# Kernel tuning notes

Measured on AMD Instinct MI355X. Metric: run time of the kernel, lower is better.

## Reference

```python
import jax, jax.numpy as jnp
import numpy as np

B, S, D = 2, 2048, 1024
H = 16
HD = D // H
W = 256  # attention window half-width


def setup_inputs() -> dict:
    key = jax.random.key(0)
    ks = jax.random.split(key, 9)
    scale = 1.0 / np.sqrt(D)
    inp = {
        "x": jax.random.normal(ks[0], (B, S, D), dtype=jnp.float32),
        "Wq": jax.random.normal(ks[1], (D, D), dtype=jnp.float32) * scale,
        "bq": jnp.zeros((D,), dtype=jnp.float32),
        "Wk": jax.random.normal(ks[2], (D, D), dtype=jnp.float32) * scale,
        "bk": jnp.zeros((D,), dtype=jnp.float32),
        "Wv": jax.random.normal(ks[3], (D, D), dtype=jnp.float32) * scale,
        "bv": jnp.zeros((D,), dtype=jnp.float32),
        "Wo": jax.random.normal(ks[4], (D, D), dtype=jnp.float32) * scale,
        "bo": jnp.zeros((D,), dtype=jnp.float32),
    }
    return inp


def reference(x, Wq, bq, Wk, bk, Wv, bv, Wo, bo):
    # Linear projections (torch Linear: x @ W.T + b), split heads -> [B,H,S,HD]
    def proj(W, b):
        y = x @ W.T + b
        return y.reshape(B, S, H, HD).transpose(0, 2, 1, 3)

    q = proj(Wq, bq)
    k = proj(Wk, bk)
    v = proj(Wv, bv)

    scores = jnp.einsum("bhqd,bhkd->bhqk", q, k) / jnp.sqrt(
        jnp.asarray(HD, dtype=jnp.float32))

    # banded local mask: keep |i - j| <= W
    i = jnp.arange(S)[:, None]
    j = jnp.arange(S)[None, :]
    local_mask = jnp.abs(i - j) <= W  # [S,S] bool
    scores = jnp.where(local_mask[None, None], scores, -jnp.inf)

    attn = jax.nn.softmax(scores, axis=-1)  # [B,H,S,S]
    context = jnp.einsum("bhqk,bhkd->bhqd", attn, v)
    context = context.transpose(0, 2, 1, 3).reshape(B, S, D)
    out = context @ Wo.T + bo
    return (out, attn)
```

## Files before the change

### kernel.cpp

```cpp
#include <hip/hip_runtime.h>

#define B_ 2
#define S_ 2048
#define D_ 1024
#define H_ 16
#define HD_ 64
#define MSZ 4096

typedef __attribute__((ext_vector_type(8))) short short8;
typedef __attribute__((ext_vector_type(4))) float f32x4;
typedef unsigned short u16;

#define MFMA16(a, b, c) __builtin_amdgcn_mfma_f32_16x16x32_bf16((a), (b), (c), 0, 0, 0)

typedef __attribute__((address_space(1))) const unsigned int gu32;
typedef __attribute__((address_space(3))) unsigned int lu32;
#define STAGE16(gp, lp) \
  __builtin_amdgcn_global_load_lds((gu32*)(gp), (lu32*)(lp), 16, 0, 0)

__device__ __forceinline__ u16 f2bf(float f) {
  union { float f; unsigned u; } v; v.f = f;
  unsigned r = v.u + 0x7FFFu + ((v.u >> 16) & 1u);
  return (u16)(r >> 16);
}
__device__ __forceinline__ float bf2f(u16 h) {
  union { unsigned u; float f; } v; v.u = ((unsigned)h) << 16;
  return v.f;
}

__global__ void split_kernel(const float* __restrict__ x, const float* __restrict__ wq,
                             const float* __restrict__ wk, const float* __restrict__ wv,
                             const float* __restrict__ wo, u16* __restrict__ xh,
                             u16* __restrict__ xl, u16* __restrict__ wch,
                             u16* __restrict__ wcl, u16* __restrict__ woh,
                             u16* __restrict__ wol) {
  const size_t base = (size_t)blockIdx.x * 256 + threadIdx.x;
#pragma unroll
  for (int it = 0; it < 4; ++it) {
    const size_t v = base + (size_t)it * 524288;
    float4 f;
    u16 *dh, *dl;
    size_t off;
    if (v < 1048576) {
      f = ((const float4*)x)[v]; dh = xh; dl = xl; off = v;
    } else if (v < 1310720) {
      f = ((const float4*)wq)[v - 1048576]; dh = wch; dl = wcl; off = v - 1048576;
    } else if (v < 1572864) {
      f = ((const float4*)wk)[v - 1310720]; dh = wch; dl = wcl; off = v - 1048576;
    } else if (v < 1835008) {
      f = ((const float4*)wv)[v - 1572864]; dh = wch; dl = wcl; off = v - 1048576;
    } else {
      f = ((const float4*)wo)[v - 1835008]; dh = woh; dl = wol; off = v - 1835008;
    }
    const float e[4] = {f.x, f.y, f.z, f.w};
    u16 h4[4], l4[4];
#pragma unroll
    for (int q = 0; q < 4; ++q) {
      h4[q] = f2bf(e[q]);
      l4[q] = f2bf(e[q] - bf2f(h4[q]));
    }
    *(ushort4*)&dh[off * 4] = make_ushort4(h4[0], h4[1], h4[2], h4[3]);
    *(ushort4*)&dl[off * 4] = make_ushort4(l4[0], l4[1], l4[2], l4[3]);
  }
}

__global__ void split_ctx(const float* __restrict__ src, u16* __restrict__ dh,
                          u16* __restrict__ dl) {
  const size_t base = (size_t)blockIdx.x * 256 + threadIdx.x;
#pragma unroll
  for (int it = 0; it < 2; ++it) {
    const size_t v = base + (size_t)it * 524288;
    float4 f = ((const float4*)src)[v];
    const float e[4] = {f.x, f.y, f.z, f.w};
    u16 h4[4], l4[4];
#pragma unroll
    for (int q = 0; q < 4; ++q) {
      h4[q] = f2bf(e[q]);
      l4[q] = f2bf(e[q] - bf2f(h4[q]));
    }
    *(ushort4*)&dh[v * 4] = make_ushort4(h4[0], h4[1], h4[2], h4[3]);
    *(ushort4*)&dl[v * 4] = make_ushort4(l4[0], l4[1], l4[2], l4[3]);
  }
}

template <int EPI>
__global__ __launch_bounds__(256, 2) void gemm_bf(
    const u16* __restrict__ Ahg, const u16* __restrict__ Alg,
    const u16* __restrict__ Bhg, const u16* __restrict__ Blg,
    const float* __restrict__ b0, const float* __restrict__ b1,
    const float* __restrict__ b2, u16* __restrict__ oh, u16* __restrict__ ol,
    float* __restrict__ outf) {
  __shared__ u16 Ah[128 * 32], Al[128 * 32], Bh[128 * 32], Bl[128 * 32];
  const int tid = threadIdx.x, lane = tid & 63, wave = tid >> 6;
  const int wr = wave >> 1, wc = wave & 1;
  const int g = lane >> 4, ln = lane & 15;
  const int mbase = blockIdx.y * 128;
  const int nbase = blockIdx.x * 128;

  f32x4 acc[4][4];
  {
    f32x4 z = {0.f, 0.f, 0.f, 0.f};
#pragma unroll
    for (int i = 0; i < 4; ++i)
#pragma unroll
      for (int j = 0; j < 4; ++j) acc[i][j] = z;
  }

  const int srow = wave * 16 + (lane >> 2);
  const int scol = (lane & 3) * 8;
  const size_t a0 = (size_t)(mbase + srow) * 1024 + scol;
  const size_t a1 = a0 + (size_t)64 * 1024;
  const size_t bo0 = (size_t)(nbase + srow) * 1024 + scol;
  const size_t bo1 = bo0 + (size_t)64 * 1024;
  u16* const lA0 = &Ah[(wave * 16) * 32];
  u16* const lA1 = &Ah[(64 + wave * 16) * 32];
  u16* const lB0 = &Bh[(wave * 16) * 32];
  u16* const lB1 = &Bh[(64 + wave * 16) * 32];
  u16* const lA0l = &Al[(wave * 16) * 32];
  u16* const lA1l = &Al[(64 + wave * 16) * 32];
  u16* const lB0l = &Bl[(wave * 16) * 32];
  u16* const lB1l = &Bl[(64 + wave * 16) * 32];

  for (int kt = 0; kt < 32; ++kt) {
    const int k0 = kt * 32;
    STAGE16(Ahg + a0 + k0, lA0);
    STAGE16(Ahg + a1 + k0, lA1);
    STAGE16(Alg + a0 + k0, lA0l);
    STAGE16(Alg + a1 + k0, lA1l);
    STAGE16(Bhg + bo0 + k0, lB0);
    STAGE16(Bhg + bo1 + k0, lB1);
    STAGE16(Blg + bo0 + k0, lB0l);
    STAGE16(Blg + bo1 + k0, lB1l);
    __syncthreads();
    short8 af[4][2], bf[4][2];
#pragma unroll
    for (int mi = 0; mi < 4; ++mi) {
      const int r = wr * 64 + mi * 16 + ln;
      af[mi][0] = *(const short8*)&Ah[r * 32 + g * 8];
      af[mi][1] = *(const short8*)&Al[r * 32 + g * 8];
    }
#pragma unroll
    for (int ni = 0; ni < 4; ++ni) {
      const int r = wc * 64 + ni * 16 + ln;
      bf[ni][0] = *(const short8*)&Bh[r * 32 + g * 8];
      bf[ni][1] = *(const short8*)&Bl[r * 32 + g * 8];
    }
#pragma unroll
    for (int mi = 0; mi < 4; ++mi)
#pragma unroll
      for (int ni = 0; ni < 4; ++ni) {
        acc[mi][ni] = MFMA16(af[mi][0], bf[ni][0], acc[mi][ni]);
        acc[mi][ni] = MFMA16(af[mi][0], bf[ni][1], acc[mi][ni]);
        acc[mi][ni] = MFMA16(af[mi][1], bf[ni][0], acc[mi][ni]);
      }
    __syncthreads();
  }

  const size_t P = (size_t)B_ * H_ * S_ * HD_;
  if constexpr (EPI == 0) {
#pragma unroll
    for (int mi = 0; mi < 4; ++mi)
#pragma unroll
      for (int ni = 0; ni < 4; ++ni) {
        const int nl3 = nbase + wc * 64 + ni * 16 + ln;
        const int which = nl3 >> 10;
        const float* bp = (which == 0) ? b0 : (which == 1) ? b1 : b2;
        const float bv = bp[nl3 & 1023];
        const int hh = (nl3 >> 6) & 15, hd = nl3 & 63;
#pragma unroll
        for (int reg = 0; reg < 4; ++reg) {
          const int mm = mbase + wr * 64 + mi * 16 + g * 4 + reg;
          const int bb = mm >> 11, ss = mm & 2047;
          const size_t dst =
              (size_t)which * P + (((size_t)bb * 16 + hh) * 2048 + ss) * 64 + hd;
          const float val = acc[mi][ni][reg] + bv;
          const u16 hi = f2bf(val);
          oh[dst] = hi;
          ol[dst] = f2bf(val - bf2f(hi));
        }
      }
  } else {
#pragma unroll
    for (int mi = 0; mi < 4; ++mi)
#pragma unroll
      for (int ni = 0; ni < 4; ++ni) {
        const int nl = nbase + wc * 64 + ni * 16 + ln;
        const float bv = b0[nl];
#pragma unroll
        for (int reg = 0; reg < 4; ++reg) {
          const int mm = mbase + wr * 64 + mi * 16 + g * 4 + reg;
          outf[(size_t)mm * 1024 + nl] = acc[mi][ni][reg] + bv;
        }
      }
  }
}

__global__ __launch_bounds__(256, 2) void attn_kernel(
    const u16* __restrict__ qh, const u16* __restrict__ ql,
    const u16* __restrict__ kh, const u16* __restrict__ kl,
    const u16* __restrict__ vh, const u16* __restrict__ vl,
    float* __restrict__ attn, float* __restrict__ ctx) {
  __shared__ u16 Plds[32][584];
  __shared__ u16 Vth[64][136], Vtl[64][136];
  __shared__ float red[2][4][32];

  const int tid = threadIdx.x, lane = tid & 63, wave = tid >> 6;
  const int g = lane >> 4, ln = lane & 15;
  int bid = blockIdx.x;
  bid = (bid & 7) * 256 + (bid >> 3);
  const int bh = bid >> 6;
  const int qblk = bid & 63;
  const int b = bh >> 4, h = bh & 15;
  const int i0 = qblk * 32;
  const int j0 = i0 - 256;
  const size_t bh_off = (size_t)bh * S_ * HD_;
  const float NINF = -__builtin_inff();

  short8 qf[2][2][2];
#pragma unroll
  for (int mi = 0; mi < 2; ++mi)
#pragma unroll
    for (int ks = 0; ks < 2; ++ks) {
      const size_t off = bh_off + (size_t)(i0 + mi * 16 + ln) * 64 + ks * 32 + g * 8;
      qf[mi][ks][0] = *(const short8*)(qh + off);
      qf[mi][ks][1] = *(const short8*)(ql + off);
    }

  f32x4 acc[2][9];
  {
    f32x4 z = {0.f, 0.f, 0.f, 0.f};
#pragma unroll
    for (int mi = 0; mi < 2; ++mi)
#pragma unroll
      for (int nn = 0; nn < 9; ++nn) acc[mi][nn] = z;
  }
#pragma unroll
  for (int nn = 0; nn < 9; ++nn) {
    const int c = wave * 144 + nn * 16 + ln;
    const int j = j0 + c;
    const int jc = min(max(j, 0), S_ - 1);
    const u16* kp = kh + bh_off + (size_t)jc * 64 + g * 8;
    const u16* lp = kl + bh_off + (size_t)jc * 64 + g * 8;
    short8 bh0 = *(const short8*)kp;
    short8 bh1 = *(const short8*)(kp + 32);
    short8 bl0 = *(const short8*)lp;
    short8 bl1 = *(const short8*)(lp + 32);
#pragma unroll
    for (int mi = 0; mi < 2; ++mi) {
      f32x4 a = acc[mi][nn];
      a = MFMA16(qf[mi][0][0], bh0, a);
      a = MFMA16(qf[mi][1][0], bh1, a);
      a = MFMA16(qf[mi][0][0], bl0, a);
      a = MFMA16(qf[mi][1][0], bl1, a);
      a = MFMA16(qf[mi][0][1], bh0, a);
      a = MFMA16(qf[mi][1][1], bh1, a);
      acc[mi][nn] = a;
    }
  }

#pragma unroll
  for (int mi = 0; mi < 2; ++mi)
#pragma unroll
    for (int nn = 0; nn < 9; ++nn) {
      const int c = wave * 144 + nn * 16 + ln;
      const int j = j0 + c;
#pragma unroll
      for (int reg = 0; reg < 4; ++reg) {
        const int r = mi * 16 + g * 4 + reg;
        const bool valid = (j >= 0) && (j < S_) && (c >= r) && (c <= r + 512);
        const float s = acc[mi][nn][reg] * 0.125f;
        acc[mi][nn][reg] = valid ? s : NINF;
      }
    }

  float rmax[2][4];
#pragma unroll
  for (int mi = 0; mi < 2; ++mi)
#pragma unroll
    for (int reg = 0; reg < 4; ++reg) {
      float m = NINF;
#pragma unroll
      for (int nn = 0; nn < 9; ++nn) m = fmaxf(m, acc[mi][nn][reg]);
#pragma unroll
      for (int msk = 1; msk < 16; msk <<= 1) m = fmaxf(m, __shfl_xor(m, msk, 64));
      rmax[mi][reg] = m;
    }
  if (ln == 0) {
#pragma unroll
    for (int mi = 0; mi < 2; ++mi)
#pragma unroll
      for (int reg = 0; reg < 4; ++reg) red[0][wave][mi * 16 + g * 4 + reg] = rmax[mi][reg];
  }
  __syncthreads();
  float gmax[2][4];
#pragma unroll
  for (int mi = 0; mi < 2; ++mi)
#pragma unroll
    for (int reg = 0; reg < 4; ++reg) {
      const int r = mi * 16 + g * 4 + reg;
      gmax[mi][reg] = fmaxf(fmaxf(red[0][0][r], red[0][1][r]), fmaxf(red[0][2][r], red[0][3][r]));
    }

  float psum[2][4];
#pragma unroll
  for (int mi = 0; mi < 2; ++mi)
#pragma unroll
    for (int reg = 0; reg < 4; ++reg) psum[mi][reg] = 0.f;
#pragma unroll
  for (int mi = 0; mi < 2; ++mi)
#pragma unroll
    for (int nn = 0; nn < 9; ++nn)
#pragma unroll
      for (int reg = 0; reg < 4; ++reg) {
        const float p = __expf(acc[mi][nn][reg] - gmax[mi][reg]);
        acc[mi][nn][reg] = p;
        psum[mi][reg] += p;
      }
#pragma unroll
  for (int mi = 0; mi < 2; ++mi)
#pragma unroll
    for (int reg = 0; reg < 4; ++reg) {
      float s = psum[mi][reg];
#pragma unroll
      for (int msk = 1; msk < 16; msk <<= 1) s += __shfl_xor(s, msk, 64);
      psum[mi][reg] = s;
    }
  if (ln == 0) {
#pragma unroll
    for (int mi = 0; mi < 2; ++mi)
#pragma unroll
      for (int reg = 0; reg < 4; ++reg) red[1][wave][mi * 16 + g * 4 + reg] = psum[mi][reg];
  }
  __syncthreads();
  float inv[2][4];
#pragma unroll
  for (int mi = 0; mi < 2; ++mi)
#pragma unroll
    for (int reg = 0; reg < 4; ++reg) {
      const int r = mi * 16 + g * 4 + reg;
      inv[mi][reg] = 1.f / (red[1][0][r] + red[1][1][r] + red[1][2][r] + red[1][3][r]);
    }

  float* attn_bh = attn + (size_t)bh * S_ * S_;
#pragma unroll
  for (int mi = 0; mi < 2; ++mi)
#pragma unroll
    for (int nn = 0; nn < 9; ++nn) {
      const int c = wave * 144 + nn * 16 + ln;
      const int j = j0 + c;
#pragma unroll
      for (int reg = 0; reg < 4; ++reg) {
        const int r = mi * 16 + g * 4 + reg;
        const float p = acc[mi][nn][reg] * inv[mi][reg];
        const bool valid = (j >= 0) && (j < S_) && (c >= r) && (c <= r + 512);
        if (valid) attn_bh[(size_t)(i0 + r) * S_ + j] = p;
        Plds[r][c] = f2bf(p);
      }
    }

  {
    const int r = tid >> 3, tt = tid & 7;
    const int i = i0 + r;
    const int lo = max(0, i - 256), hi = min(S_ - 1, i + 256);
    float* rowp = attn_bh + (size_t)i * S_;
    const float4 z4 = make_float4(0.f, 0.f, 0.f, 0.f);
    const int lo4 = lo >> 2;
    for (int x = tt; x < lo4; x += 8) ((float4*)rowp)[x] = z4;
    if (tt == 0)
      for (int jj = lo & ~3; jj < lo; ++jj) rowp[jj] = 0.f;
    const int t0 = hi + 1;
    int t4 = (t0 + 3) & ~3;
    if (t4 > S_) t4 = S_;
    if (tt == 1)
      for (int jj = t0; jj < t4; ++jj) rowp[jj] = 0.f;
    for (int x = (t4 >> 2) + tt; x < S_ / 4; x += 8) ((float4*)rowp)[x] = z4;
  }
  __syncthreads();

  f32x4 ctxa[2];
  {
    f32x4 z = {0.f, 0.f, 0.f, 0.f};
    ctxa[0] = z;
    ctxa[1] = z;
  }
  const int a2 = ((wave * 16 + ln) >> 3) & 3;
  for (int ch = 0; ch < 5; ++ch) {
    const int cw = (ch == 4) ? 64 : 128;
    for (int u = tid; u < cw * 8; u += 256) {
      const int cc = u >> 3, hd0 = (u & 7) * 8;
      const int sw = (u & 3) << 3;
      const int j = j0 + ch * 128 + cc;
      const int jc = min(max(j, 0), S_ - 1);
      short8 v8 = *(const short8*)(vh + bh_off + (size_t)jc * 64 + hd0);
      short8 w8 = *(const short8*)(vl + bh_off + (size_t)jc * 64 + hd0);
      const int cs = cc ^ sw;
#pragma unroll
      for (int e = 0; e < 8; ++e) {
        Vth[hd0 + e][cs] = (u16)v8[e];
        Vtl[hd0 + e][cs] = (u16)w8[e];
      }
    }
    __syncthreads();
    const int nks = cw >> 5;
    for (int ks = 0; ks < nks; ++ks) {
      const int kc = ks * 32 + g * 8;
      const int kcs = kc ^ (a2 << 3);
      short8 vbh = *(const short8*)&Vth[wave * 16 + ln][kcs];
      short8 vbl = *(const short8*)&Vtl[wave * 16 + ln][kcs];
#pragma unroll
      for (int mi = 0; mi < 2; ++mi) {
        short8 pa = *(const short8*)&Plds[mi * 16 + ln][ch * 128 + kc];
        ctxa[mi] = MFMA16(pa, vbh, ctxa[mi]);
        ctxa[mi] = MFMA16(pa, vbl, ctxa[mi]);
      }
    }
    __syncthreads();
  }

#pragma unroll
  for (int mi = 0; mi < 2; ++mi)
#pragma unroll
    for (int reg = 0; reg < 4; ++reg) {
      const int r = mi * 16 + g * 4 + reg;
      const int d = wave * 16 + ln;
      ctx[(size_t)(b * S_ + i0 + r) * 1024 + h * 64 + d] = ctxa[mi][reg];
    }
}

extern "C" void kernel_launch(void* const* d_in, const int* in_sizes, int n_in,
                              void* d_out, int out_size, void* d_ws, size_t ws_size,
                              hipStream_t stream) {
  (void)in_sizes; (void)n_in; (void)out_size; (void)ws_size;
  const float* x  = (const float*)d_in[0];
  const float* Wq = (const float*)d_in[1];
  const float* bq = (const float*)d_in[2];
  const float* Wk = (const float*)d_in[3];
  const float* bk = (const float*)d_in[4];
  const float* Wv = (const float*)d_in[5];
  const float* bv = (const float*)d_in[6];
  const float* Wo = (const float*)d_in[7];
  const float* bo = (const float*)d_in[8];
  float* out = (float*)d_out;
  float* attn = out + (size_t)B_ * S_ * D_;

  const size_t P = (size_t)B_ * H_ * S_ * HD_;
  u16* qkvh = (u16*)d_ws;
  u16* qkvl = qkvh + 3 * P;
  float* ctx = (float*)(qkvl + 3 * P);
  u16* xh = (u16*)(ctx + (size_t)MSZ * 1024);
  u16* xl = xh + (size_t)MSZ * 1024;
  u16* wch = xl + (size_t)MSZ * 1024;
  u16* wcl = wch + 3145728;
  u16* woh = wcl + 3145728;
  u16* wol = woh + 1048576;
  u16* ch  = wol + 1048576;
  u16* cl  = ch + (size_t)MSZ * 1024;

  split_kernel<<<2048, 256, 0, stream>>>(x, Wq, Wk, Wv, Wo, xh, xl, wch, wcl, woh, wol);

  dim3 g1(24, 32);
  gemm_bf<0><<<g1, 256, 0, stream>>>(xh, xl, wch, wcl, bq, bk, bv,
                                     qkvh, qkvl, nullptr);

  attn_kernel<<<2048, 256, 0, stream>>>(qkvh, qkvl, qkvh + P, qkvl + P,
                                        qkvh + 2 * P, qkvl + 2 * P, attn, ctx);

  split_ctx<<<2048, 256, 0, stream>>>(ctx, ch, cl);

  dim3 g3(8, 32);
  gemm_bf<1><<<g3, 256, 0, stream>>>(ch, cl, woh, wol, bo, bo, bo,
                                     nullptr, nullptr, out);
}
```

Baseline: 802.3 us.

## Drop low bf16 parts of K/V, skip softmax max, prefetch V, nontemporal stores

```diff
diff --git a/kernel.cpp b/kernel.cpp
--- a/kernel.cpp
+++ b/kernel.cpp
@@ -197,12 +197,11 @@
 
 __global__ __launch_bounds__(256, 2) void attn_kernel(
     const u16* __restrict__ qh, const u16* __restrict__ ql,
-    const u16* __restrict__ kh, const u16* __restrict__ kl,
-    const u16* __restrict__ vh, const u16* __restrict__ vl,
+    const u16* __restrict__ kh, const u16* __restrict__ vh,
     float* __restrict__ attn, float* __restrict__ ctx) {
   __shared__ u16 Plds[32][584];
-  __shared__ u16 Vth[64][136], Vtl[64][136];
-  __shared__ float red[2][4][32];
+  __shared__ u16 Vth[64][136];
+  __shared__ float red[4][32];
 
   const int tid = threadIdx.x, lane = tid & 63, wave = tid >> 6;
   const int g = lane >> 4, ln = lane & 15;
@@ -214,7 +213,6 @@
   const int i0 = qblk * 32;
   const int j0 = i0 - 256;
   const size_t bh_off = (size_t)bh * S_ * HD_;
-  const float NINF = -__builtin_inff();
 
   short8 qf[2][2][2];
 #pragma unroll
@@ -240,24 +238,34 @@
     const int j = j0 + c;
     const int jc = min(max(j, 0), S_ - 1);
     const u16* kp = kh + bh_off + (size_t)jc * 64 + g * 8;
-    const u16* lp = kl + bh_off + (size_t)jc * 64 + g * 8;
-    short8 bh0 = *(const short8*)kp;
-    short8 bh1 = *(const short8*)(kp + 32);
-    short8 bl0 = *(const short8*)lp;
-    short8 bl1 = *(const short8*)(lp + 32);
+    short8 kh0 = *(const short8*)kp;
+    short8 kh1 = *(const short8*)(kp + 32);
 #pragma unroll
     for (int mi = 0; mi < 2; ++mi) {
       f32x4 a = acc[mi][nn];
-      a = MFMA16(qf[mi][0][0], bh0, a);
-      a = MFMA16(qf[mi][1][0], bh1, a);
-      a = MFMA16(qf[mi][0][0], bl0, a);
-      a = MFMA16(qf[mi][1][0], bl1, a);
-      a = MFMA16(qf[mi][0][1], bh0, a);
-      a = MFMA16(qf[mi][1][1], bh1, a);
+      a = MFMA16(qf[mi][0][0], kh0, a);
+      a = MFMA16(qf[mi][1][0], kh1, a);
+      a = MFMA16(qf[mi][0][1], kh0, a);
+      a = MFMA16(qf[mi][1][1], kh1, a);
       acc[mi][nn] = a;
     }
   }
 
+  short8 vreg[4];
+#pragma unroll
+  for (int it = 0; it < 4; ++it) {
+    const int u = tid + it * 256;
+    const int cc = u >> 3, hd0 = (u & 7) * 8;
+    const int j = j0 + cc;
+    const int jc = min(max(j, 0), S_ - 1);
+    vreg[it] = *(const short8*)(vh + bh_off + (size_t)jc * 64 + hd0);
+  }
+
+  float psum[2][4];
+#pragma unroll
+  for (int mi = 0; mi < 2; ++mi)
+#pragma unroll
+    for (int reg = 0; reg < 4; ++reg) psum[mi][reg] = 0.f;
 #pragma unroll
   for (int mi = 0; mi < 2; ++mi)
 #pragma unroll
@@ -268,80 +276,121 @@
       for (int reg = 0; reg < 4; ++reg) {
         const int r = mi * 16 + g * 4 + reg;
         const bool valid = (j >= 0) && (j < S_) && (c >= r) && (c <= r + 512);
-        const float s = acc[mi][nn][reg] * 0.125f;
-        acc[mi][nn][reg] = valid ? s : NINF;
-      }
-    }
-
-  float rmax[2][4];
+        const float p = valid ? __expf(acc[mi][nn][reg] * 0.125f) : 0.f;
+        acc[mi][nn][reg] = p;
+        psum[mi][reg] += p;
+      }
+    }
 #pragma unroll
   for (int mi = 0; mi < 2; ++mi)
 #pragma unroll
     for (int reg = 0; reg < 4; ++reg) {
-      float m = NINF;
-#pragma unroll
-      for (int nn = 0; nn < 9; ++nn) m = fmaxf(m, acc[mi][nn][reg]);
-#pragma unroll
-      for (int msk = 1; msk < 16; msk <<= 1) m = fmaxf(m, __shfl_xor(m, msk, 64));
-      rmax[mi][reg] = m;
+      float s = psum[mi][reg];
+#pragma unroll
+      for (int msk = 1; msk < 16; msk <<= 1) s += __shfl_xor(s, msk, 64);
+      psum[mi][reg] = s;
     }
   if (ln == 0) {
 #pragma unroll
     for (int mi = 0; mi < 2; ++mi)
 #pragma unroll
-      for (int reg = 0; reg < 4; ++reg) red[0][wave][mi * 16 + g * 4 + reg] = rmax[mi][reg];
-  }
+      for (int reg = 0; reg < 4; ++reg) red[wave][mi * 16 + g * 4 + reg] = psum[mi][reg];
+  }
+
+#pragma unroll
+  for (int mi = 0; mi < 2; ++mi)
+#pragma unroll
+    for (int nn = 0; nn < 9; ++nn) {
+      const int c = wave * 144 + nn * 16 + ln;
+#pragma unroll
+      for (int reg = 0; reg < 4; ++reg)
+        Plds[mi * 16 + g * 4 + reg][c] = f2bf(acc[mi][nn][reg]);
+    }
   __syncthreads();
-  float gmax[2][4];
+
+  float inv[2][4];
 #pragma unroll
   for (int mi = 0; mi < 2; ++mi)
 #pragma unroll
     for (int reg = 0; reg < 4; ++reg) {
       const int r = mi * 16 + g * 4 + reg;
-      gmax[mi][reg] = fmaxf(fmaxf(red[0][0][r], red[0][1][r]), fmaxf(red[0][2][r], red[0][3][r]));
-    }
-
-  float psum[2][4];
-#pragma unroll
-  for (int mi = 0; mi < 2; ++mi)
-#pragma unroll
-    for (int reg = 0; reg < 4; ++reg) psum[mi][reg] = 0.f;
-#pragma unroll
-  for (int mi = 0; mi < 2; ++mi)
-#pragma unroll
-    for (int nn = 0; nn < 9; ++nn)
-#pragma unroll
-      for (int reg = 0; reg < 4; ++reg) {
-        const float p = __expf(acc[mi][nn][reg] - gmax[mi][reg]);
-        acc[mi][nn][reg] = p;
-        psum[mi][reg] += p;
-      }
-#pragma unroll
-  for (int mi = 0; mi < 2; ++mi)
-#pragma unroll
-    for (int reg = 0; reg < 4; ++reg) {
-      float s = psum[mi][reg];
-#pragma unroll
-      for (int msk = 1; msk < 16; msk <<= 1) s += __shfl_xor(s, msk, 64);
-      psum[mi][reg] = s;
-    }
-  if (ln == 0) {
-#pragma unroll
-    for (int mi = 0; mi < 2; ++mi)
-#pragma unroll
-      for (int reg = 0; reg < 4; ++reg) red[1][wave][mi * 16 + g * 4 + reg] = psum[mi][reg];
+      inv[mi][reg] = 1.f / (red[0][r] + red[1][r] + red[2][r] + red[3][r]);
+    }
+
+#pragma unroll
+  for (int it = 0; it < 4; ++it) {
+    const int u = tid + it * 256;
+    const int cc = u >> 3, hd0 = (u & 7) * 8;
+    const int cs = cc ^ ((u & 3) << 3);
+#pragma unroll
+    for (int e = 0; e < 8; ++e) Vth[hd0 + e][cs] = (u16)vreg[it][e];
   }
   __syncthreads();
-  float inv[2][4];
+
+  f32x4 ctxa[2];
+  {
+    f32x4 z = {0.f, 0.f, 0.f, 0.f};
+    ctxa[0] = z;
+    ctxa[1] = z;
+  }
+  const int a2 = ((wave * 16 + ln) >> 3) & 3;
+#pragma unroll
+  for (int ch = 0; ch < 5; ++ch) {
+    const int cw = (ch == 4) ? 64 : 128;
+    if (ch < 4) {
+      const int cw2 = (ch == 3) ? 64 : 128;
+#pragma unroll
+      for (int it = 0; it < 4; ++it) {
+        const int u = tid + it * 256;
+        if (u < cw2 * 8) {
+          const int cc = u >> 3, hd0 = (u & 7) * 8;
+          const int j = j0 + (ch + 1) * 128 + cc;
+          const int jc = min(max(j, 0), S_ - 1);
+          vreg[it] = *(const short8*)(vh + bh_off + (size_t)jc * 64 + hd0);
+        }
+      }
+    }
+    const int nks = cw >> 5;
+    for (int ks = 0; ks < nks; ++ks) {
+      const int kc = ks * 32 + g * 8;
+      const int kcs = kc ^ (a2 << 3);
+      short8 vb = *(const short8*)&Vth[wave * 16 + ln][kcs];
+#pragma unroll
+      for (int mi = 0; mi < 2; ++mi) {
+        short8 pa = *(const short8*)&Plds[mi * 16 + ln][ch * 128 + kc];
+        ctxa[mi] = MFMA16(pa, vb, ctxa[mi]);
+      }
+    }
+    if (ch < 4) {
+      __syncthreads();
+      const int cw2 = (ch == 3) ? 64 : 128;
+#pragma unroll
+      for (int it = 0; it < 4; ++it) {
+        const int u = tid + it * 256;
+        if (u < cw2 * 8) {
+          const int cc = u >> 3, hd0 = (u & 7) * 8;
+          const int cs = cc ^ ((u & 3) << 3);
+#pragma unroll
+          for (int e = 0; e < 8; ++e) Vth[hd0 + e][cs] = (u16)vreg[it][e];
+        }
+      }
+      __syncthreads();
+    }
+  }
+
+  float* attn_bh = attn + (size_t)bh * S_ * S_;
+
 #pragma unroll
   for (int mi = 0; mi < 2; ++mi)
 #pragma unroll
     for (int reg = 0; reg < 4; ++reg) {
       const int r = mi * 16 + g * 4 + reg;
-      inv[mi][reg] = 1.f / (red[1][0][r] + red[1][1][r] + red[1][2][r] + red[1][3][r]);
-    }
-
-  float* attn_bh = attn + (size_t)bh * S_ * S_;
+      const int d = wave * 16 + ln;
+      __builtin_nontemporal_store(
+          ctxa[mi][reg] * inv[mi][reg],
+          &ctx[(size_t)(b * S_ + i0 + r) * 1024 + h * 64 + d]);
+    }
+
 #pragma unroll
   for (int mi = 0; mi < 2; ++mi)
 #pragma unroll
@@ -351,10 +400,10 @@
 #pragma unroll
       for (int reg = 0; reg < 4; ++reg) {
         const int r = mi * 16 + g * 4 + reg;
-        const float p = acc[mi][nn][reg] * inv[mi][reg];
         const bool valid = (j >= 0) && (j < S_) && (c >= r) && (c <= r + 512);
-        if (valid) attn_bh[(size_t)(i0 + r) * S_ + j] = p;
-        Plds[r][c] = f2bf(p);
+        if (valid)
+          __builtin_nontemporal_store(acc[mi][nn][reg] * inv[mi][reg],
+                                      &attn_bh[(size_t)(i0 + r) * S_ + j]);
       }
     }
 
@@ -363,68 +412,22 @@
     const int i = i0 + r;
     const int lo = max(0, i - 256), hi = min(S_ - 1, i + 256);
     float* rowp = attn_bh + (size_t)i * S_;
-    const float4 z4 = make_float4(0.f, 0.f, 0.f, 0.f);
+    const f32x4 z4 = {0.f, 0.f, 0.f, 0.f};
     const int lo4 = lo >> 2;
-    for (int x = tt; x < lo4; x += 8) ((float4*)rowp)[x] = z4;
+    for (int x = tt; x < lo4; x += 8)
+      __builtin_nontemporal_store(z4, (f32x4*)rowp + x);
     if (tt == 0)
-      for (int jj = lo & ~3; jj < lo; ++jj) rowp[jj] = 0.f;
+      for (int jj = lo & ~3; jj < lo; ++jj)
+        __builtin_nontemporal_store(0.f, rowp + jj);
     const int t0 = hi + 1;
     int t4 = (t0 + 3) & ~3;
     if (t4 > S_) t4 = S_;
     if (tt == 1)
-      for (int jj = t0; jj < t4; ++jj) rowp[jj] = 0.f;
-    for (int x = (t4 >> 2) + tt; x < S_ / 4; x += 8) ((float4*)rowp)[x] = z4;
-  }
-  __syncthreads();
-
-  f32x4 ctxa[2];
-  {
-    f32x4 z = {0.f, 0.f, 0.f, 0.f};
-    ctxa[0] = z;
-    ctxa[1] = z;
-  }
-  const int a2 = ((wave * 16 + ln) >> 3) & 3;
-  for (int ch = 0; ch < 5; ++ch) {
-    const int cw = (ch == 4) ? 64 : 128;
-    for (int u = tid; u < cw * 8; u += 256) {
-      const int cc = u >> 3, hd0 = (u & 7) * 8;
-      const int sw = (u & 3) << 3;
-      const int j = j0 + ch * 128 + cc;
-      const int jc = min(max(j, 0), S_ - 1);
-      short8 v8 = *(const short8*)(vh + bh_off + (size_t)jc * 64 + hd0);
-      short8 w8 = *(const short8*)(vl + bh_off + (size_t)jc * 64 + hd0);
-      const int cs = cc ^ sw;
-#pragma unroll
-      for (int e = 0; e < 8; ++e) {
-        Vth[hd0 + e][cs] = (u16)v8[e];
-        Vtl[hd0 + e][cs] = (u16)w8[e];
-      }
-    }
-    __syncthreads();
-    const int nks = cw >> 5;
-    for (int ks = 0; ks < nks; ++ks) {
-      const int kc = ks * 32 + g * 8;
-      const int kcs = kc ^ (a2 << 3);
-      short8 vbh = *(const short8*)&Vth[wave * 16 + ln][kcs];
-      short8 vbl = *(const short8*)&Vtl[wave * 16 + ln][kcs];
-#pragma unroll
-      for (int mi = 0; mi < 2; ++mi) {
-        short8 pa = *(const short8*)&Plds[mi * 16 + ln][ch * 128 + kc];
-        ctxa[mi] = MFMA16(pa, vbh, ctxa[mi]);
-        ctxa[mi] = MFMA16(pa, vbl, ctxa[mi]);
-      }
-    }
-    __syncthreads();
-  }
-
-#pragma unroll
-  for (int mi = 0; mi < 2; ++mi)
-#pragma unroll
-    for (int reg = 0; reg < 4; ++reg) {
-      const int r = mi * 16 + g * 4 + reg;
-      const int d = wave * 16 + ln;
-      ctx[(size_t)(b * S_ + i0 + r) * 1024 + h * 64 + d] = ctxa[mi][reg];
-    }
+      for (int jj = t0; jj < t4; ++jj)
+        __builtin_nontemporal_store(0.f, rowp + jj);
+    for (int x = (t4 >> 2) + tt; x < S_ / 4; x += 8)
+      __builtin_nontemporal_store(z4, (f32x4*)rowp + x);
+  }
 }
 
 extern "C" void kernel_launch(void* const* d_in, const int* in_sizes, int n_in,
@@ -462,8 +465,8 @@
   gemm_bf<0><<<g1, 256, 0, stream>>>(xh, xl, wch, wcl, bq, bk, bv,
                                      qkvh, qkvl, nullptr);
 
-  attn_kernel<<<2048, 256, 0, stream>>>(qkvh, qkvl, qkvh + P, qkvl + P,
-                                        qkvh + 2 * P, qkvl + 2 * P, attn, ctx);
+  attn_kernel<<<2048, 256, 0, stream>>>(qkvh, qkvl, qkvh + P,
+                                        qkvh + 2 * P, attn, ctx);
 
   split_ctx<<<2048, 256, 0, stream>>>(ctx, ch, cl);
 
```

After: 811.8 us. Within noise of the previous version (+1.2%).
